# Optimization experiments

Hardware: AMD Instinct MI355X
Metric: run time of the kernel (lower is better)

The kernel has to match this reference:

```python
import jax, jax.numpy as jnp
import numpy as np

N = 100000        # nodes
E = 3200000       # edges
IN = 256          # in_feats
H = 8             # num_heads
O = 64            # out_feats
F = 64            # edge_feats
T = 8             # num_etypes

def setup_inputs() -> dict:
    key = jax.random.key(0)
    ks = jax.random.split(key, 10)
    return {
        "feat": jax.random.normal(ks[0], (N, IN), jnp.float32) * 0.1,
        "etype": jax.random.randint(ks[1], (E,), 0, T, jnp.int32),
        "src": jax.random.randint(ks[2], (E,), 0, N, jnp.int32),
        "dst": jax.random.randint(ks[3], (E,), 0, N, jnp.int32),
        "W_fc": jax.random.normal(ks[4], (IN, H * O), jnp.float32) * (1.0 / np.sqrt(IN)),
        "edge_emb": jax.random.normal(ks[5], (T, F), jnp.float32),
        "W_e": jax.random.normal(ks[6], (F, H * F), jnp.float32) * (1.0 / np.sqrt(F)),
        "attn_l": jax.random.normal(ks[7], (H, O), jnp.float32) * 0.1,
        "attn_r": jax.random.normal(ks[8], (H, O), jnp.float32) * 0.1,
        "attn_e": jax.random.normal(ks[9], (H, F), jnp.float32) * 0.1,
    }

def reference(feat, etype, src, dst, W_fc, edge_emb, W_e, attn_l, attn_r, attn_e):
    n = feat.shape[0]
    # node projection + per-head attention logits
    h = (feat @ W_fc).reshape(n, H, O)                      # [N,H,O]
    el = jnp.einsum('nho,ho->nh', h, attn_l)                # [N,H]
    er = jnp.einsum('nho,ho->nh', h, attn_r)                # [N,H]
    # edge-type embedding -> projection -> logit (project the tiny table once, then gather)
    emb_proj = (edge_emb @ W_e).reshape(T, H, F)            # [T,H,F]
    ee = jnp.einsum('thf,hf->th', emb_proj, attn_e)[etype]  # [E,H]
    # u_add_v + edge bias, then ReLU (module's "leaky_relu" is nn.ReLU())
    e = jax.nn.relu(el[src] + er[dst] + ee)                 # [E,H]
    # segment softmax grouped by destination node
    m = jax.ops.segment_max(e, dst, num_segments=n)         # [N,H]
    ex = jnp.exp(e - m[dst])                                # [E,H]
    s = jax.ops.segment_sum(ex, dst, num_segments=n)        # [N,H]
    return ex / s[dst]                                      # [E,H]
```

## Files before the change

kernel.cpp:

```cpp
#include <hip/hip_runtime.h>
#include <math.h>

#define NN 100000
#define NE 3200000
#define INF_ 256
#define NH 8
#define OF 64
#define EF 64
#define NT 8

#define BSH 7
#define BNODES 128
#define NB 782
#define CAPB 4608
#define SPLIT 4
#define EPB 4096

static constexpr size_t WS_AT      = 0;
static constexpr size_t WS_EE      = 4096;
static constexpr size_t WS_EL      = 4160;
static constexpr size_t WS_ERS     = WS_EL + (size_t)NN * 8;
static constexpr size_t WS_CCNT    = WS_ERS + (size_t)NN * 16;
static constexpr size_t WS_PART    = WS_CCNT + NB + 2;

__global__ __launch_bounds__(256) void k_prep_A(const float* __restrict__ W_fc,
                                                const float* __restrict__ attn_l,
                                                const float* __restrict__ attn_r,
                                                float* __restrict__ At,
                                                unsigned* __restrict__ ccnt) {
    int t = blockIdx.x * 256 + threadIdx.x;
    if (t < NB) ccnt[t] = 0u;
    int c = t >> 8;
    int i = t & 255;
    int h = c & 7;
    const float* attn = (c < 8) ? attn_l : attn_r;
    const float* wrow = W_fc + (size_t)i * (NH * OF) + h * OF;
    const float* arow = attn + h * OF;
    float acc = 0.f;
#pragma unroll 8
    for (int o = 0; o < OF; ++o) acc += wrow[o] * arow[o];
    At[c * INF_ + i] = acc;
}

__global__ __launch_bounds__(512) void k_prep_ee(const float* __restrict__ edge_emb,
                                                 const float* __restrict__ W_e,
                                                 const float* __restrict__ attn_e,
                                                 float* __restrict__ ee_tab) {
    __shared__ float B[EF][NH];
    int t = threadIdx.x;
    int g = t >> 3, h = t & 7;
    const float* wrow = W_e + (size_t)g * (NH * EF) + h * EF;
    const float* arow = attn_e + h * EF;
    float acc = 0.f;
#pragma unroll 8
    for (int f = 0; f < EF; ++f) acc += wrow[f] * arow[f];
    B[g][h] = acc;
    __syncthreads();
    if (t < NT * NH) {
        int tt = t >> 3, hh = t & 7;
        float a = 0.f;
#pragma unroll 8
        for (int g2 = 0; g2 < EF; ++g2) a += edge_emb[tt * EF + g2] * B[g2][hh];
        ee_tab[tt * NH + hh] = a;
    }
}

__global__ __launch_bounds__(256) void k_node(const float* __restrict__ feat,
                                              const float* __restrict__ At,
                                              float* __restrict__ el,
                                              float* __restrict__ ers) {
    int n = blockIdx.x * 256 + threadIdx.x;
    if (n >= NN) return;
    const float4* f4 = (const float4*)(feat + (size_t)n * INF_);
    const float4* A4 = (const float4*)At;
    float acc[16];
#pragma unroll
    for (int c = 0; c < 16; ++c) acc[c] = 0.f;
    for (int iq = 0; iq < INF_ / 4; ++iq) {
        float4 f = f4[iq];
#pragma unroll
        for (int c = 0; c < 16; ++c) {
            float4 a = A4[c * 64 + iq];
            acc[c] += f.x * a.x + f.y * a.y + f.z * a.z + f.w * a.w;
        }
    }
    float4* e4 = (float4*)(el + (size_t)n * 8);
    e4[0] = make_float4(acc[0], acc[1], acc[2], acc[3]);
    e4[1] = make_float4(acc[4], acc[5], acc[6], acc[7]);
    float4* r4 = (float4*)(ers + (size_t)n * 16);
    r4[0] = make_float4(acc[8], acc[9], acc[10], acc[11]);
    r4[1] = make_float4(acc[12], acc[13], acc[14], acc[15]);
    r4[2] = make_float4(0.f, 0.f, 0.f, 0.f);
    r4[3] = make_float4(0.f, 0.f, 0.f, 0.f);
}

__global__ __launch_bounds__(256) void k_partition(const int* __restrict__ src,
                                                   const int* __restrict__ dst,
                                                   const int* __restrict__ etype,
                                                   unsigned* __restrict__ ccnt,
                                                   unsigned* __restrict__ part) {
    __shared__ unsigned hist[NB];
    __shared__ unsigned cursor[NB];
    int tid = threadIdx.x;
    size_t base = (size_t)blockIdx.x * EPB;
    unsigned long long rc[16];
    for (int i = tid; i < NB; i += 256) hist[i] = 0u;
    __syncthreads();
#pragma unroll
    for (int k = 0; k < 16; ++k) {
        size_t j = base + (size_t)k * 256 + tid;
        if (j < NE) {
            int dj = dst[j];
            rc[k] = (unsigned long long)(unsigned)src[j]
                  | ((unsigned long long)(unsigned)etype[j] << 17)
                  | ((unsigned long long)(unsigned)dj << 20);
            atomicAdd(&hist[dj >> BSH], 1u);
        } else rc[k] = ~0ull;
    }
    __syncthreads();
    for (int i = tid; i < NB; i += 256) {
        unsigned h = hist[i];
        cursor[i] = h ? atomicAdd(ccnt + i, h) : 0u;
    }
    __syncthreads();
#pragma unroll
    for (int k = 0; k < 16; ++k) {
        if (rc[k] == ~0ull) continue;
        int dj = (int)(rc[k] >> 20);
        int b = dj >> BSH;
        unsigned pos = atomicAdd(&cursor[b], 1u);
        if (pos < CAPB)
            part[(size_t)b * CAPB + pos] =
                (unsigned)(rc[k] & 0xFFFFFull) | ((unsigned)(dj & (BNODES - 1)) << 20);
    }
}

__global__ __launch_bounds__(256) void k_bucket_sum(const unsigned* __restrict__ part,
                                                    const unsigned* __restrict__ ccnt,
                                                    const float* __restrict__ el,
                                                    const float* __restrict__ ers,
                                                    const float* __restrict__ ee_tab,
                                                    float* __restrict__ ers_out) {
    __shared__ float sbin[BNODES * 9];
    __shared__ float er_l[BNODES * 9];
    __shared__ float ee_l[NT * NH];
    int bs = blockIdx.x;
    int b = bs >> 2, c = bs & 3;
    int tid = threadIdx.x;
    int e_sub = tid >> 3, h = tid & 7;
    int n0 = b << BSH;
    int nn = NN - n0; if (nn > BNODES) nn = BNODES;

    for (int i = tid; i < BNODES * 9; i += 256) sbin[i] = 0.f;
    if (tid < NT * NH) ee_l[tid] = ee_tab[tid];
    for (int i = tid; i < nn * NH; i += 256) {
        int nl = i >> 3, hh = i & 7;
        er_l[nl * 9 + hh] = ers[(size_t)(n0 + nl) * 16 + hh];
    }
    __syncthreads();

    unsigned cnt = ccnt[b]; if (cnt > CAPB) cnt = CAPB;
    const unsigned* pp = part + (size_t)b * CAPB;
    unsigned e = (unsigned)(c * 32 + e_sub);
    for (; e + 896 < cnt; e += 1024) {
        unsigned r0 = pp[e];
        unsigned r1 = pp[e + 128];
        unsigned r2 = pp[e + 256];
        unsigned r3 = pp[e + 384];
        unsigned r4 = pp[e + 512];
        unsigned r5 = pp[e + 640];
        unsigned r6 = pp[e + 768];
        unsigned r7 = pp[e + 896];
        float l0 = el[(size_t)(r0 & 0x1FFFFu) * 8 + h];
        float l1 = el[(size_t)(r1 & 0x1FFFFu) * 8 + h];
        float l2 = el[(size_t)(r2 & 0x1FFFFu) * 8 + h];
        float l3 = el[(size_t)(r3 & 0x1FFFFu) * 8 + h];
        float l4 = el[(size_t)(r4 & 0x1FFFFu) * 8 + h];
        float l5 = el[(size_t)(r5 & 0x1FFFFu) * 8 + h];
        float l6 = el[(size_t)(r6 & 0x1FFFFu) * 8 + h];
        float l7 = el[(size_t)(r7 & 0x1FFFFu) * 8 + h];
#define DO_EDGE(rr, ll)                                                        \
        {                                                                      \
            int et = (int)(((rr) >> 17) & 7u);                                 \
            int dl = (int)(((rr) >> 20) & (BNODES - 1));                       \
            float v = (ll) + er_l[dl * 9 + h] + ee_l[et * NH + h];             \
            atomicAdd(&sbin[dl * 9 + h], __expf(fmaxf(v, 0.f)));               \
        }
        DO_EDGE(r0, l0)
        DO_EDGE(r1, l1)
        DO_EDGE(r2, l2)
        DO_EDGE(r3, l3)
        DO_EDGE(r4, l4)
        DO_EDGE(r5, l5)
        DO_EDGE(r6, l6)
        DO_EDGE(r7, l7)
    }
    for (; e < cnt; e += 128) {
        unsigned rec = pp[e];
        float lv = el[(size_t)(rec & 0x1FFFFu) * 8 + h];
        DO_EDGE(rec, lv)
    }
#undef DO_EDGE
    __syncthreads();
    for (int i = tid; i < nn * NH; i += 256) {
        int nl = i >> 3, hh = i & 7;
        atomicAdd(&ers_out[(size_t)(n0 + nl) * 16 + 8 + hh], sbin[nl * 9 + hh]);
    }
}

__global__ __launch_bounds__(256) void k_edge_out(const int* __restrict__ src,
                                                  const int* __restrict__ dst,
                                                  const int* __restrict__ etype,
                                                  const float* __restrict__ el,
                                                  const float* __restrict__ ers,
                                                  const float* __restrict__ ee_tab,
                                                  float* __restrict__ out) {
    int j = blockIdx.x * 256 + threadIdx.x;
    if (j >= NE) return;
    int sj = src[j], dj = dst[j], tj = etype[j];
    const float4* el4 = (const float4*)(el + (size_t)sj * 8);
    const float4* E   = (const float4*)(ers + (size_t)dj * 16);
    const float4* ee4 = (const float4*)(ee_tab + tj * NH);
    float4 l0 = el4[0], l1 = el4[1];
    float4 r0 = E[0], r1 = E[1];
    float4 s0 = E[2], s1 = E[3];
    float4 e0 = ee4[0], e1 = ee4[1];
    float4 o0, o1;
    o0.x = __expf(fmaxf(l0.x + r0.x + e0.x, 0.f)) / s0.x;
    o0.y = __expf(fmaxf(l0.y + r0.y + e0.y, 0.f)) / s0.y;
    o0.z = __expf(fmaxf(l0.z + r0.z + e0.z, 0.f)) / s0.z;
    o0.w = __expf(fmaxf(l0.w + r0.w + e0.w, 0.f)) / s0.w;
    o1.x = __expf(fmaxf(l1.x + r1.x + e1.x, 0.f)) / s1.x;
    o1.y = __expf(fmaxf(l1.y + r1.y + e1.y, 0.f)) / s1.y;
    o1.z = __expf(fmaxf(l1.z + r1.z + e1.z, 0.f)) / s1.z;
    o1.w = __expf(fmaxf(l1.w + r1.w + e1.w, 0.f)) / s1.w;
    float4* o4 = (float4*)(out + (size_t)j * NH);
    o4[0] = o0;
    o4[1] = o1;
}

extern "C" void kernel_launch(void* const* d_in, const int* in_sizes, int n_in,
                              void* d_out, int out_size, void* d_ws, size_t ws_size,
                              hipStream_t stream) {
    const float* feat     = (const float*)d_in[0];
    const int*   etype    = (const int*)d_in[1];
    const int*   src      = (const int*)d_in[2];
    const int*   dst      = (const int*)d_in[3];
    const float* W_fc     = (const float*)d_in[4];
    const float* edge_emb = (const float*)d_in[5];
    const float* W_e      = (const float*)d_in[6];
    const float* attn_l   = (const float*)d_in[7];
    const float* attn_r   = (const float*)d_in[8];
    const float* attn_e   = (const float*)d_in[9];

    float*    ws      = (float*)d_ws;
    float*    At      = ws + WS_AT;
    float*    ee_tab  = ws + WS_EE;
    float*    el      = ws + WS_EL;
    float*    ers     = ws + WS_ERS;
    unsigned* ccnt    = (unsigned*)(ws + WS_CCNT);
    unsigned* part    = (unsigned*)(ws + WS_PART);
    float*    out     = (float*)d_out;

    hipLaunchKernelGGL(k_prep_A, dim3(16), dim3(256), 0, stream, W_fc, attn_l, attn_r, At, ccnt);
    hipLaunchKernelGGL(k_prep_ee, dim3(1), dim3(512), 0, stream, edge_emb, W_e, attn_e, ee_tab);
    hipLaunchKernelGGL(k_node, dim3((NN + 255) / 256), dim3(256), 0, stream, feat, At, el, ers);
    hipLaunchKernelGGL(k_partition, dim3((NE + EPB - 1) / EPB), dim3(256), 0, stream,
                       src, dst, etype, ccnt, part);
    hipLaunchKernelGGL(k_bucket_sum, dim3(NB * SPLIT), dim3(256), 0, stream,
                       part, ccnt, el, ers, ee_tab, ers);
    hipLaunchKernelGGL(k_edge_out, dim3((NE + 255) / 256), dim3(256), 0, stream,
                       src, dst, etype, el, ers, ee_tab, out);
}
```

Measured before the change: 523.9 us.

## Map one edge per thread with float4 loads in bucket sum kernel

Changes k_bucket_sum from eight threads per edge (one per head) to one thread per edge handling all eight heads. The thread reads el, the destination er and the edge-type bias as float4 vectors from global memory instead of staging er and ee in shared memory. This cuts the per-edge record loads and scalar el gathers and removes the shared staging. In exchange each thread issues eight LDS atomics that hit the same node row, which can raise bank conflicts, and the manual 8-way unroll for memory-level parallelism is dropped.

```diff
diff --git a/kernel.cpp b/kernel.cpp
--- a/kernel.cpp
+++ b/kernel.cpp
@@ -142,65 +142,38 @@
                                                     const float* __restrict__ ee_tab,
                                                     float* __restrict__ ers_out) {
     __shared__ float sbin[BNODES * 9];
-    __shared__ float er_l[BNODES * 9];
-    __shared__ float ee_l[NT * NH];
     int bs = blockIdx.x;
     int b = bs >> 2, c = bs & 3;
     int tid = threadIdx.x;
-    int e_sub = tid >> 3, h = tid & 7;
     int n0 = b << BSH;
     int nn = NN - n0; if (nn > BNODES) nn = BNODES;
 
     for (int i = tid; i < BNODES * 9; i += 256) sbin[i] = 0.f;
-    if (tid < NT * NH) ee_l[tid] = ee_tab[tid];
-    for (int i = tid; i < nn * NH; i += 256) {
-        int nl = i >> 3, hh = i & 7;
-        er_l[nl * 9 + hh] = ers[(size_t)(n0 + nl) * 16 + hh];
-    }
     __syncthreads();
 
     unsigned cnt = ccnt[b]; if (cnt > CAPB) cnt = CAPB;
     const unsigned* pp = part + (size_t)b * CAPB;
-    unsigned e = (unsigned)(c * 32 + e_sub);
-    for (; e + 896 < cnt; e += 1024) {
-        unsigned r0 = pp[e];
-        unsigned r1 = pp[e + 128];
-        unsigned r2 = pp[e + 256];
-        unsigned r3 = pp[e + 384];
-        unsigned r4 = pp[e + 512];
-        unsigned r5 = pp[e + 640];
-        unsigned r6 = pp[e + 768];
-        unsigned r7 = pp[e + 896];
-        float l0 = el[(size_t)(r0 & 0x1FFFFu) * 8 + h];
-        float l1 = el[(size_t)(r1 & 0x1FFFFu) * 8 + h];
-        float l2 = el[(size_t)(r2 & 0x1FFFFu) * 8 + h];
-        float l3 = el[(size_t)(r3 & 0x1FFFFu) * 8 + h];
-        float l4 = el[(size_t)(r4 & 0x1FFFFu) * 8 + h];
-        float l5 = el[(size_t)(r5 & 0x1FFFFu) * 8 + h];
-        float l6 = el[(size_t)(r6 & 0x1FFFFu) * 8 + h];
-        float l7 = el[(size_t)(r7 & 0x1FFFFu) * 8 + h];
-#define DO_EDGE(rr, ll)                                                        \
-        {                                                                      \
-            int et = (int)(((rr) >> 17) & 7u);                                 \
-            int dl = (int)(((rr) >> 20) & (BNODES - 1));                       \
-            float v = (ll) + er_l[dl * 9 + h] + ee_l[et * NH + h];             \
-            atomicAdd(&sbin[dl * 9 + h], __expf(fmaxf(v, 0.f)));               \
-        }
-        DO_EDGE(r0, l0)
-        DO_EDGE(r1, l1)
-        DO_EDGE(r2, l2)
-        DO_EDGE(r3, l3)
-        DO_EDGE(r4, l4)
-        DO_EDGE(r5, l5)
-        DO_EDGE(r6, l6)
-        DO_EDGE(r7, l7)
-    }
-    for (; e < cnt; e += 128) {
+    for (unsigned e = (unsigned)(c * 256 + tid); e < cnt; e += 1024) {
         unsigned rec = pp[e];
-        float lv = el[(size_t)(rec & 0x1FFFFu) * 8 + h];
-        DO_EDGE(rec, lv)
-    }
-#undef DO_EDGE
+        int sj = (int)(rec & 0x1FFFFu);
+        int et = (int)((rec >> 17) & 7u);
+        int dl = (int)((rec >> 20) & (BNODES - 1));
+        const float4* el4 = (const float4*)(el + (size_t)sj * 8);
+        const float4* E   = (const float4*)(ers + (size_t)(n0 + dl) * 16);
+        const float4* ee4 = (const float4*)(ee_tab + et * NH);
+        float4 la = el4[0], lb = el4[1];
+        float4 ra = E[0],   rb = E[1];
+        float4 ea = ee4[0], eb = ee4[1];
+        float* sb = &sbin[dl * 9];
+        atomicAdd(&sb[0], __expf(fmaxf(la.x + ra.x + ea.x, 0.f)));
+        atomicAdd(&sb[1], __expf(fmaxf(la.y + ra.y + ea.y, 0.f)));
+        atomicAdd(&sb[2], __expf(fmaxf(la.z + ra.z + ea.z, 0.f)));
+        atomicAdd(&sb[3], __expf(fmaxf(la.w + ra.w + ea.w, 0.f)));
+        atomicAdd(&sb[4], __expf(fmaxf(lb.x + rb.x + eb.x, 0.f)));
+        atomicAdd(&sb[5], __expf(fmaxf(lb.y + rb.y + eb.y, 0.f)));
+        atomicAdd(&sb[6], __expf(fmaxf(lb.z + rb.z + eb.z, 0.f)));
+        atomicAdd(&sb[7], __expf(fmaxf(lb.w + rb.w + eb.w, 0.f)));
+    }
     __syncthreads();
     for (int i = tid; i < nn * NH; i += 256) {
         int nl = i >> 3, hh = i & 7;
```

New measurement: 519.6 us. About the same (-0.8%).
